# Kernel optimization log

Measured on AMD Instinct MI355X. Metric: run time of the kernel, lower is better.

## Reference

```python
import jax, jax.numpy as jnp
import numpy as np

LRELU_GAIN = np.sqrt(2.0).astype(np.float32)  # apply_activation gain for leaky_relu


def setup_inputs() -> dict:
    key = jax.random.key(0)
    ks = jax.random.split(key, 8)
    N, H, W, C_in = 8, 256, 256, 128
    num_ws, w_dim, fmaps, kernel = 16, 512, 128, 3
    return {
        "x": jax.random.normal(ks[0], (N, H, W, C_in), dtype=jnp.float32),
        "dlatents": jax.random.normal(ks[1], (N, num_ws, w_dim), dtype=jnp.float32),
        "noise": jax.random.normal(ks[2], (N, H, W, 1), dtype=jnp.float32),
        "affine_w": jax.random.normal(ks[3], (w_dim, C_in), dtype=jnp.float32),
        "affine_b": jnp.ones((C_in,), dtype=jnp.float32),  # bias_init=1
        "conv_w": jax.random.normal(ks[4], (kernel, kernel, C_in, fmaps), dtype=jnp.float32),
        "conv_b": jax.random.normal(ks[5], (fmaps,), dtype=jnp.float32),
        "noise_strength": jax.random.uniform(ks[6], (1,), dtype=jnp.float32),
        "layer_idx": 5,
    }


def reference(x, dlatents, noise, affine_w, affine_b, conv_w, conv_b, noise_strength, layer_idx):
    # --- affine (equalized-lr Linear, lr_multiplier=1): s = z @ (W/sqrt(fan_in)) + b ---
    w_dim = affine_w.shape[0]
    z = dlatents[:, layer_idx]                                   # [N, w_dim]
    s = z @ (affine_w * np.float32(1.0 / np.sqrt(w_dim))) + affine_b   # [N, C_in]

    # --- equalized-lr conv weight: w * 1/sqrt(k*k*C_in) ---
    k, _, cin, cout = conv_w.shape
    w = conv_w * np.float32(1.0 / np.sqrt(k * k * cin))          # [k,k,Cin,Cout]

    # --- demodulation coefficient d[n,o] = rsqrt(sum_{k,k,i} (w*s)^2 + eps) ---
    d = jax.lax.rsqrt(jnp.einsum('hwio,ni->no', jnp.square(w), jnp.square(s)) + 1e-8)  # [N, Cout]

    # --- non-fused modconv: modulate input, shared conv, demodulate output ---
    xm = x * s[:, None, None, :]                                 # [N,H,W,Cin]
    y = jax.lax.conv_general_dilated(
        xm, w, window_strides=(1, 1), padding='SAME',
        dimension_numbers=('NHWC', 'HWIO', 'NHWC'))              # [N,H,W,Cout]
    y = y * d[:, None, None, :]

    # --- noise injection, bias, activation (leaky_relu 0.2 with sqrt(2) gain) ---
    y = y + noise_strength[0] * noise
    y = y + conv_b
    return jax.nn.leaky_relu(y, negative_slope=0.2) * LRELU_GAIN
```

## Files before the change

### kernel.cpp

```cpp
#include <hip/hip_runtime.h>

typedef unsigned short u16;
typedef unsigned int   u32;
typedef __bf16 v8bf __attribute__((ext_vector_type(8)));
typedef float  v4f  __attribute__((ext_vector_type(4)));

#define INV_SQRT_W   0.044194173824159216f
#define INV_SQRT_KKC 0.029462782549439483f
#define LRELU_GAIN   1.4142135623730951f

__device__ __forceinline__ u16 f2bf(float f) {
    u32 u = __float_as_uint(f);
    u = (u + 0x7fffu + ((u >> 16) & 1u)) >> 16;
    return (u16)u;
}

__device__ __forceinline__ void glds16(const u16* g, u16* l) {
    __builtin_amdgcn_global_load_lds(
        (const __attribute__((address_space(1))) void*)g,
        (__attribute__((address_space(3))) void*)l, 16, 0, 0);
}

__global__ void k_s1(const float* __restrict__ dlat,
                     const float* __restrict__ aw,
                     const int*   __restrict__ lidx,
                     float* __restrict__ part)
{
    const int b   = blockIdx.x;
    const int n   = b >> 2, kh = b & 3;
    const int tid = threadIdx.x;
    const int i   = tid & 127, half = tid >> 7;
    const int li  = lidx[0];
    const float* z = dlat + (n * 16 + li) * 512 + kh * 128 + half * 64;
    const float* a = aw + (kh * 128 + half * 64) * 128 + i;
    float a0 = 0.f, a1 = 0.f;
    #pragma unroll 8
    for (int k = 0; k < 64; k += 2) {
        a0 += z[k]     * a[k * 128];
        a1 += z[k + 1] * a[(k + 1) * 128];
    }
    __shared__ float red[256];
    red[tid] = a0 + a1;
    __syncthreads();
    if (tid < 128)
        part[b * 128 + i] = red[i] + red[i + 128];
}

__global__ void k_s2(const float* __restrict__ part,
                     const float* __restrict__ ab,
                     float* __restrict__ s_out)
{
    const int n = blockIdx.x, i = threadIdx.x;
    float s = part[(n * 4 + 0) * 128 + i] + part[(n * 4 + 1) * 128 + i]
            + part[(n * 4 + 2) * 128 + i] + part[(n * 4 + 3) * 128 + i];
    s_out[n * 128 + i] = s * INV_SQRT_W + ab[i];
}

__global__ void k_w2(const float* __restrict__ cw, float* __restrict__ W2)
{
    const int idx = blockIdx.x * 256 + threadIdx.x;
    float acc = 0.f;
    #pragma unroll
    for (int t = 0; t < 9; ++t) {
        float w = cw[t * 16384 + idx];
        acc += w * w;
    }
    W2[idx] = acc * (INV_SQRT_KKC * INV_SQRT_KKC);
}

__global__ void k_d(const float* __restrict__ W2,
                    const float* __restrict__ s_buf,
                    float* __restrict__ d_out)
{
    const int n = blockIdx.x;
    const int o = threadIdx.x;
    __shared__ float s2[128];
    float sv = s_buf[n * 128 + o];
    s2[o] = sv * sv;
    __syncthreads();
    float acc = 1e-8f;
    #pragma unroll 4
    for (int i = 0; i < 128; ++i)
        acc += W2[i * 128 + o] * s2[i];
    d_out[n * 128 + o] = 1.0f / sqrtf(acc);
}

__global__ void k_wmod(const float* __restrict__ cw,
                       const float* __restrict__ s_buf,
                       const float* __restrict__ d_buf,
                       u16* __restrict__ wmod)
{
    const int b   = blockIdx.x;
    const int n   = b / 36;
    const int s   = b - n * 36;
    const int q4  = s / 9;
    const int r   = s - q4 * 9;
    const int tw  = r / 3, th = r - tw * 3;
    const int tap = th * 3 + tw;
    const int cibase = q4 * 32;
    const int tid = threadIdx.x;
    __shared__ float ssh[32], dsh[128];
    if (tid < 32)  ssh[tid] = s_buf[n * 128 + cibase + tid] * INV_SQRT_KKC;
    if (tid < 128) dsh[tid] = d_buf[n * 128 + tid];
    __syncthreads();
    u16* wt = wmod + ((size_t)b << 12);
    #pragma unroll
    for (int rep = 0; rep < 2; ++rep) {
        int t2   = rep * 256 + tid;
        int g    = t2 >> 7;
        int cout = t2 & 127;
        float dv = dsh[cout];
        u32 pk[4];
        #pragma unroll
        for (int jj = 0; jj < 4; ++jj) {
            int cl = g * 8 + jj * 2;
            float v0 = cw[((tap * 128 + cibase + cl) << 7) + cout]     * ssh[cl]     * dv;
            float v1 = cw[((tap * 128 + cibase + cl + 1) << 7) + cout] * ssh[cl + 1] * dv;
            pk[jj] = (u32)f2bf(v0) | ((u32)f2bf(v1) << 16);
        }
        *(uint4*)&wt[(g << 10) + (cout << 3)] = *(uint4*)pk;
    }
}

template<int T>
__device__ __forceinline__ void conv_step(const u16* __restrict__ wn,
                                          u16* __restrict__ bsh,
                                          const u16* a_base,
                                          const u16* b_lane,
                                          v8bf af[6], v4f acc[4][4],
                                          int wid, int lane)
{
    constexpr int q4 = T / 9, r = T % 9, tw = r / 3, th = r % 3;
    constexpr int slot = T % 3;
    constexpr int hq = q4 & 1;
    if constexpr (T == 0 || T == 18)
        asm volatile("s_waitcnt vmcnt(1) lgkmcnt(0)" ::: "memory");
    else if constexpr (T == 35)
        asm volatile("s_waitcnt vmcnt(0)" ::: "memory");
    else
        asm volatile("s_waitcnt vmcnt(1)" ::: "memory");
    __builtin_amdgcn_s_barrier();
    asm volatile("" ::: "memory");

    v8bf bf[4];
    #pragma unroll
    for (int ni = 0; ni < 4; ++ni)
        bf[ni] = *(const v8bf*)(b_lane + slot * 4096 + (ni << 7));
    if constexpr (th == 0) {
        #pragma unroll
        for (int j = 0; j < 6; ++j)
            af[j] = *(const v8bf*)(a_base + hq * 10400 + (j * 18 + tw) * 8);
    }
    if constexpr (T + 2 < 36) {
        constexpr int ns = (T + 2) % 3;
        glds16(wn + (T + 2) * 4096 + (wid << 9) + (lane << 3),
               &bsh[ns * 4096 + (wid << 9) + (lane << 3)]);
    }
    #pragma unroll
    for (int mi = 0; mi < 4; ++mi)
        #pragma unroll
        for (int ni = 0; ni < 4; ++ni)
            acc[mi][ni] = __builtin_amdgcn_mfma_f32_16x16x32_bf16(
                af[mi + th], bf[ni], acc[mi][ni], 0, 0, 0);
}

__global__ __launch_bounds__(512, 4) void k_conv(
    const float* __restrict__ x,
    const float* __restrict__ noise,
    const float* __restrict__ conv_b,
    const float* __restrict__ nstr,
    const u16*   __restrict__ wmod,
    float* __restrict__ out)
{
    __shared__ __align__(16) u16 xs[20800];
    __shared__ __align__(16) u16 bsh[12288];

    const int bid0 = blockIdx.x;
    const int bid  = ((bid0 & 7) << 8) + (bid0 >> 3);
    const int n   = bid >> 8;
    const int hb  = (bid >> 4) & 15;
    const int wb  = bid & 15;
    const int h0  = hb << 4, w0 = wb << 4;

    const int tid  = threadIdx.x;
    const int lane = tid & 63;
    const int wid  = tid >> 6;
    const int wm   = wid >> 1;
    const int wn_  = wid & 1;
    const int lr   = lane & 15;
    const int kg   = lane >> 4;

    const float* xbase = x + ((size_t)n << 16) * 128;

    #define STAGE_X(ph)                                                              \
    for (int t = tid; t < 2592; t += 512) {                                          \
        int q = t >> 3, g = t & 7;                                                   \
        int rr_ = q / 18, cc = q - rr_ * 18;                                         \
        int gh = h0 + rr_ - 1, gw = w0 + cc - 1;                                     \
        float v0=0.f,v1=0.f,v2=0.f,v3=0.f,v4=0.f,v5=0.f,v6=0.f,v7=0.f;               \
        if ((unsigned)gh < 256u && (unsigned)gw < 256u) {                            \
            const float* src = xbase + (size_t)((gh << 8) + gw) * 128                \
                               + (ph) * 64 + (g << 3);                               \
            float4 fa = *(const float4*)(src);                                       \
            float4 fb = *(const float4*)(src + 4);                                   \
            v0=fa.x; v1=fa.y; v2=fa.z; v3=fa.w; v4=fb.x; v5=fb.y; v6=fb.z; v7=fb.w;  \
        }                                                                            \
        v8bf pk;                                                                     \
        pk[0]=(__bf16)v0; pk[1]=(__bf16)v1; pk[2]=(__bf16)v2; pk[3]=(__bf16)v3;      \
        pk[4]=(__bf16)v4; pk[5]=(__bf16)v5; pk[6]=(__bf16)v6; pk[7]=(__bf16)v7;      \
        *(v8bf*)&xs[g * 2600 + q * 8] = pk;                                          \
    }

    STAGE_X(0)

    const u16* wn = wmod + ((size_t)n * 36) * 4096;
    #pragma unroll
    for (int s0 = 0; s0 < 2; ++s0)
        glds16(wn + s0 * 4096 + (wid << 9) + (lane << 3),
               &bsh[s0 * 4096 + (wid << 9) + (lane << 3)]);

    v4f acc[4][4];
    #pragma unroll
    for (int a = 0; a < 4; ++a)
        #pragma unroll
        for (int b2 = 0; b2 < 4; ++b2) {
            v4f zz = {0.f, 0.f, 0.f, 0.f};
            acc[a][b2] = zz;
        }

    const u16* const a_base = &xs[kg * 2600 + (wm * 72 + lr) * 8];
    const u16* const b_lane = &bsh[kg * 1024 + (wn_ * 64 + lr) * 8];

    v8bf af[6];
    conv_step< 0>(wn, bsh, a_base, b_lane, af, acc, wid, lane);
    conv_step< 1>(wn, bsh, a_base, b_lane, af, acc, wid, lane);
    conv_step< 2>(wn, bsh, a_base, b_lane, af, acc, wid, lane);
    conv_step< 3>(wn, bsh, a_base, b_lane, af, acc, wid, lane);
    conv_step< 4>(wn, bsh, a_base, b_lane, af, acc, wid, lane);
    conv_step< 5>(wn, bsh, a_base, b_lane, af, acc, wid, lane);
    conv_step< 6>(wn, bsh, a_base, b_lane, af, acc, wid, lane);
    conv_step< 7>(wn, bsh, a_base, b_lane, af, acc, wid, lane);
    conv_step< 8>(wn, bsh, a_base, b_lane, af, acc, wid, lane);
    conv_step< 9>(wn, bsh, a_base, b_lane, af, acc, wid, lane);
    conv_step<10>(wn, bsh, a_base, b_lane, af, acc, wid, lane);
    conv_step<11>(wn, bsh, a_base, b_lane, af, acc, wid, lane);
    conv_step<12>(wn, bsh, a_base, b_lane, af, acc, wid, lane);
    conv_step<13>(wn, bsh, a_base, b_lane, af, acc, wid, lane);
    conv_step<14>(wn, bsh, a_base, b_lane, af, acc, wid, lane);
    conv_step<15>(wn, bsh, a_base, b_lane, af, acc, wid, lane);
    conv_step<16>(wn, bsh, a_base, b_lane, af, acc, wid, lane);
    conv_step<17>(wn, bsh, a_base, b_lane, af, acc, wid, lane);

    STAGE_X(1)

    conv_step<18>(wn, bsh, a_base, b_lane, af, acc, wid, lane);
    conv_step<19>(wn, bsh, a_base, b_lane, af, acc, wid, lane);
    conv_step<20>(wn, bsh, a_base, b_lane, af, acc, wid, lane);
    conv_step<21>(wn, bsh, a_base, b_lane, af, acc, wid, lane);
    conv_step<22>(wn, bsh, a_base, b_lane, af, acc, wid, lane);
    conv_step<23>(wn, bsh, a_base, b_lane, af, acc, wid, lane);
    conv_step<24>(wn, bsh, a_base, b_lane, af, acc, wid, lane);
    conv_step<25>(wn, bsh, a_base, b_lane, af, acc, wid, lane);
    conv_step<26>(wn, bsh, a_base, b_lane, af, acc, wid, lane);
    conv_step<27>(wn, bsh, a_base, b_lane, af, acc, wid, lane);
    conv_step<28>(wn, bsh, a_base, b_lane, af, acc, wid, lane);
    conv_step<29>(wn, bsh, a_base, b_lane, af, acc, wid, lane);
    conv_step<30>(wn, bsh, a_base, b_lane, af, acc, wid, lane);
    conv_step<31>(wn, bsh, a_base, b_lane, af, acc, wid, lane);
    conv_step<32>(wn, bsh, a_base, b_lane, af, acc, wid, lane);
    conv_step<33>(wn, bsh, a_base, b_lane, af, acc, wid, lane);
    conv_step<34>(wn, bsh, a_base, b_lane, af, acc, wid, lane);
    conv_step<35>(wn, bsh, a_base, b_lane, af, acc, wid, lane);

    const float ns = nstr[0];
    float cb4[4];
    #pragma unroll
    for (int ni = 0; ni < 4; ++ni)
        cb4[ni] = conv_b[wn_ * 64 + ni * 16 + lr];
    #pragma unroll
    for (int mi = 0; mi < 4; ++mi) {
        const int h = h0 + wm * 4 + mi;
        #pragma unroll
        for (int j = 0; j < 4; ++j) {
            const int w  = w0 + kg * 4 + j;
            const float nz = noise[((n << 8) + h) * 256 + w] * ns;
            float* orow = out + (size_t)((((n << 8) + h) << 8) + w) * 128;
            #pragma unroll
            for (int ni = 0; ni < 4; ++ni) {
                const int cout = wn_ * 64 + ni * 16 + lr;
                float v = acc[mi][ni][j] + nz + cb4[ni];
                v = (v < 0.f ? 0.2f * v : v) * LRELU_GAIN;
                orow[cout] = v;
            }
        }
    }
}

extern "C" void kernel_launch(void* const* d_in, const int* in_sizes, int n_in,
                              void* d_out, int out_size, void* d_ws, size_t ws_size,
                              hipStream_t stream) {
    const float* x     = (const float*)d_in[0];
    const float* dlat  = (const float*)d_in[1];
    const float* noise = (const float*)d_in[2];
    const float* aw    = (const float*)d_in[3];
    const float* ab    = (const float*)d_in[4];
    const float* cw    = (const float*)d_in[5];
    const float* cb    = (const float*)d_in[6];
    const float* nstr  = (const float*)d_in[7];
    const int*   lidx  = (const int*)d_in[8];
    float* out = (float*)d_out;

    float* s_buf = (float*)d_ws;
    float* d_buf = (float*)((char*)d_ws + 4096);
    float* W2    = (float*)((char*)d_ws + 8192);
    u16*   wmod  = (u16*)((char*)d_ws + 8192);
    float* part  = (float*)((char*)d_ws + 8192 + 2359296);

    k_w2  <<<64,  256, 0, stream>>>(cw, W2);
    k_s1  <<<32,  256, 0, stream>>>(dlat, aw, lidx, part);
    k_s2  <<<8,   128, 0, stream>>>(part, ab, s_buf);
    k_d   <<<8,   128, 0, stream>>>(W2, s_buf, d_buf);
    k_wmod<<<288, 256, 0, stream>>>(cw, s_buf, d_buf, wmod);
    k_conv<<<2048,512, 0, stream>>>(x, noise, cb, nstr, wmod, out);
}
```

Baseline: 195.0 us.

## Prefetch next stage's LDS fragments before barrier and raise MFMA priority

Restructures the conv main loop so each step issues its global-to-LDS weight prefetch, runs the MFMAs at raised wave priority, then waits, barriers and loads the next stage's A/B fragments into registers. The goal is to take the LDS reads and the barrier off the critical path just before the MFMAs, so matrix work overlaps fragment loading. The prologue now issues three weight stages, one of which is loaded again redundantly by step 0, and barriers are placed explicitly around the x restaging. The waitcnt bookkeeping is more delicate, and holding the next stage's fragments in registers during the MFMAs raises register pressure.

Measured after the change: 197.2 us. No clear change (+1.2%).

```diff
diff --git a/kernel.cpp b/kernel.cpp
--- a/kernel.cpp
+++ b/kernel.cpp
@@ -122,27 +122,14 @@
     }
 }
 
-template<int T>
-__device__ __forceinline__ void conv_step(const u16* __restrict__ wn,
-                                          u16* __restrict__ bsh,
-                                          const u16* a_base,
-                                          const u16* b_lane,
-                                          v8bf af[6], v4f acc[4][4],
-                                          int wid, int lane)
-{
-    constexpr int q4 = T / 9, r = T % 9, tw = r / 3, th = r % 3;
-    constexpr int slot = T % 3;
-    constexpr int hq = q4 & 1;
-    if constexpr (T == 0 || T == 18)
-        asm volatile("s_waitcnt vmcnt(1) lgkmcnt(0)" ::: "memory");
-    else if constexpr (T == 35)
-        asm volatile("s_waitcnt vmcnt(0)" ::: "memory");
-    else
-        asm volatile("s_waitcnt vmcnt(1)" ::: "memory");
-    __builtin_amdgcn_s_barrier();
-    asm volatile("" ::: "memory");
-
-    v8bf bf[4];
+template<int S>
+__device__ __forceinline__ void read_stage(const u16* __restrict__ b_lane,
+                                           const u16* __restrict__ a_base,
+                                           v8bf bf[4], v8bf af[6])
+{
+    constexpr int slot = S % 3;
+    constexpr int r = S % 9, tw = r / 3, th = r % 3;
+    constexpr int hq = (S / 9) & 1;
     #pragma unroll
     for (int ni = 0; ni < 4; ++ni)
         bf[ni] = *(const v8bf*)(b_lane + slot * 4096 + (ni << 7));
@@ -151,17 +138,41 @@
         for (int j = 0; j < 6; ++j)
             af[j] = *(const v8bf*)(a_base + hq * 10400 + (j * 18 + tw) * 8);
     }
+}
+
+template<int T, bool DO_TAIL>
+__device__ __forceinline__ void conv_step(const u16* __restrict__ wn,
+                                          u16* __restrict__ bsh,
+                                          const u16* __restrict__ a_base,
+                                          const u16* __restrict__ b_lane,
+                                          v8bf af[6], v8bf bf[4],
+                                          v4f acc[4][4],
+                                          int wid, int lane)
+{
+    constexpr int th = (T % 9) % 3;
     if constexpr (T + 2 < 36) {
         constexpr int ns = (T + 2) % 3;
         glds16(wn + (T + 2) * 4096 + (wid << 9) + (lane << 3),
                &bsh[ns * 4096 + (wid << 9) + (lane << 3)]);
     }
+    asm volatile("s_waitcnt lgkmcnt(0)" ::: "memory");
+    __builtin_amdgcn_s_setprio(1);
     #pragma unroll
     for (int mi = 0; mi < 4; ++mi)
         #pragma unroll
         for (int ni = 0; ni < 4; ++ni)
             acc[mi][ni] = __builtin_amdgcn_mfma_f32_16x16x32_bf16(
                 af[mi + th], bf[ni], acc[mi][ni], 0, 0, 0);
+    __builtin_amdgcn_s_setprio(0);
+    if constexpr (DO_TAIL) {
+        if constexpr (T + 2 < 36)
+            asm volatile("s_waitcnt vmcnt(1)" ::: "memory");
+        else
+            asm volatile("s_waitcnt vmcnt(0)" ::: "memory");
+        __builtin_amdgcn_s_barrier();
+        asm volatile("" ::: "memory");
+        read_stage<T + 1>(b_lane, a_base, bf, af);
+    }
 }
 
 __global__ __launch_bounds__(512, 4) void k_conv(
@@ -215,7 +226,7 @@
 
     const u16* wn = wmod + ((size_t)n * 36) * 4096;
     #pragma unroll
-    for (int s0 = 0; s0 < 2; ++s0)
+    for (int s0 = 0; s0 < 3; ++s0)
         glds16(wn + s0 * 4096 + (wid << 9) + (lane << 3),
                &bsh[s0 * 4096 + (wid << 9) + (lane << 3)]);
 
@@ -231,46 +242,59 @@
     const u16* const a_base = &xs[kg * 2600 + (wm * 72 + lr) * 8];
     const u16* const b_lane = &bsh[kg * 1024 + (wn_ * 64 + lr) * 8];
 
-    v8bf af[6];
-    conv_step< 0>(wn, bsh, a_base, b_lane, af, acc, wid, lane);
-    conv_step< 1>(wn, bsh, a_base, b_lane, af, acc, wid, lane);
-    conv_step< 2>(wn, bsh, a_base, b_lane, af, acc, wid, lane);
-    conv_step< 3>(wn, bsh, a_base, b_lane, af, acc, wid, lane);
-    conv_step< 4>(wn, bsh, a_base, b_lane, af, acc, wid, lane);
-    conv_step< 5>(wn, bsh, a_base, b_lane, af, acc, wid, lane);
-    conv_step< 6>(wn, bsh, a_base, b_lane, af, acc, wid, lane);
-    conv_step< 7>(wn, bsh, a_base, b_lane, af, acc, wid, lane);
-    conv_step< 8>(wn, bsh, a_base, b_lane, af, acc, wid, lane);
-    conv_step< 9>(wn, bsh, a_base, b_lane, af, acc, wid, lane);
-    conv_step<10>(wn, bsh, a_base, b_lane, af, acc, wid, lane);
-    conv_step<11>(wn, bsh, a_base, b_lane, af, acc, wid, lane);
-    conv_step<12>(wn, bsh, a_base, b_lane, af, acc, wid, lane);
-    conv_step<13>(wn, bsh, a_base, b_lane, af, acc, wid, lane);
-    conv_step<14>(wn, bsh, a_base, b_lane, af, acc, wid, lane);
-    conv_step<15>(wn, bsh, a_base, b_lane, af, acc, wid, lane);
-    conv_step<16>(wn, bsh, a_base, b_lane, af, acc, wid, lane);
-    conv_step<17>(wn, bsh, a_base, b_lane, af, acc, wid, lane);
+    asm volatile("s_waitcnt vmcnt(2) lgkmcnt(0)" ::: "memory");
+    __builtin_amdgcn_s_barrier();
+    asm volatile("" ::: "memory");
+    v8bf af[6], bf[4];
+    read_stage<0>(b_lane, a_base, bf, af);
+
+    conv_step< 0, true >(wn, bsh, a_base, b_lane, af, bf, acc, wid, lane);
+    conv_step< 1, true >(wn, bsh, a_base, b_lane, af, bf, acc, wid, lane);
+    conv_step< 2, true >(wn, bsh, a_base, b_lane, af, bf, acc, wid, lane);
+    conv_step< 3, true >(wn, bsh, a_base, b_lane, af, bf, acc, wid, lane);
+    conv_step< 4, true >(wn, bsh, a_base, b_lane, af, bf, acc, wid, lane);
+    conv_step< 5, true >(wn, bsh, a_base, b_lane, af, bf, acc, wid, lane);
+    conv_step< 6, true >(wn, bsh, a_base, b_lane, af, bf, acc, wid, lane);
+    conv_step< 7, true >(wn, bsh, a_base, b_lane, af, bf, acc, wid, lane);
+    conv_step< 8, true >(wn, bsh, a_base, b_lane, af, bf, acc, wid, lane);
+    conv_step< 9, true >(wn, bsh, a_base, b_lane, af, bf, acc, wid, lane);
+    conv_step<10, true >(wn, bsh, a_base, b_lane, af, bf, acc, wid, lane);
+    conv_step<11, true >(wn, bsh, a_base, b_lane, af, bf, acc, wid, lane);
+    conv_step<12, true >(wn, bsh, a_base, b_lane, af, bf, acc, wid, lane);
+    conv_step<13, true >(wn, bsh, a_base, b_lane, af, bf, acc, wid, lane);
+    conv_step<14, true >(wn, bsh, a_base, b_lane, af, bf, acc, wid, lane);
+    conv_step<15, true >(wn, bsh, a_base, b_lane, af, bf, acc, wid, lane);
+    conv_step<16, true >(wn, bsh, a_base, b_lane, af, bf, acc, wid, lane);
+    conv_step<17, false>(wn, bsh, a_base, b_lane, af, bf, acc, wid, lane);
+    asm volatile("s_waitcnt vmcnt(1)" ::: "memory");
+    __builtin_amdgcn_s_barrier();
+    asm volatile("" ::: "memory");
 
     STAGE_X(1)
 
-    conv_step<18>(wn, bsh, a_base, b_lane, af, acc, wid, lane);
-    conv_step<19>(wn, bsh, a_base, b_lane, af, acc, wid, lane);
-    conv_step<20>(wn, bsh, a_base, b_lane, af, acc, wid, lane);
-    conv_step<21>(wn, bsh, a_base, b_lane, af, acc, wid, lane);
-    conv_step<22>(wn, bsh, a_base, b_lane, af, acc, wid, lane);
-    conv_step<23>(wn, bsh, a_base, b_lane, af, acc, wid, lane);
-    conv_step<24>(wn, bsh, a_base, b_lane, af, acc, wid, lane);
-    conv_step<25>(wn, bsh, a_base, b_lane, af, acc, wid, lane);
-    conv_step<26>(wn, bsh, a_base, b_lane, af, acc, wid, lane);
-    conv_step<27>(wn, bsh, a_base, b_lane, af, acc, wid, lane);
-    conv_step<28>(wn, bsh, a_base, b_lane, af, acc, wid, lane);
-    conv_step<29>(wn, bsh, a_base, b_lane, af, acc, wid, lane);
-    conv_step<30>(wn, bsh, a_base, b_lane, af, acc, wid, lane);
-    conv_step<31>(wn, bsh, a_base, b_lane, af, acc, wid, lane);
-    conv_step<32>(wn, bsh, a_base, b_lane, af, acc, wid, lane);
-    conv_step<33>(wn, bsh, a_base, b_lane, af, acc, wid, lane);
-    conv_step<34>(wn, bsh, a_base, b_lane, af, acc, wid, lane);
-    conv_step<35>(wn, bsh, a_base, b_lane, af, acc, wid, lane);
+    asm volatile("s_waitcnt lgkmcnt(0)" ::: "memory");
+    __builtin_amdgcn_s_barrier();
+    asm volatile("" ::: "memory");
+    read_stage<18>(b_lane, a_base, bf, af);
+
+    conv_step<18, true >(wn, bsh, a_base, b_lane, af, bf, acc, wid, lane);
+    conv_step<19, true >(wn, bsh, a_base, b_lane, af, bf, acc, wid, lane);
+    conv_step<20, true >(wn, bsh, a_base, b_lane, af, bf, acc, wid, lane);
+    conv_step<21, true >(wn, bsh, a_base, b_lane, af, bf, acc, wid, lane);
+    conv_step<22, true >(wn, bsh, a_base, b_lane, af, bf, acc, wid, lane);
+    conv_step<23, true >(wn, bsh, a_base, b_lane, af, bf, acc, wid, lane);
+    conv_step<24, true >(wn, bsh, a_base, b_lane, af, bf, acc, wid, lane);
+    conv_step<25, true >(wn, bsh, a_base, b_lane, af, bf, acc, wid, lane);
+    conv_step<26, true >(wn, bsh, a_base, b_lane, af, bf, acc, wid, lane);
+    conv_step<27, true >(wn, bsh, a_base, b_lane, af, bf, acc, wid, lane);
+    conv_step<28, true >(wn, bsh, a_base, b_lane, af, bf, acc, wid, lane);
+    conv_step<29, true >(wn, bsh, a_base, b_lane, af, bf, acc, wid, lane);
+    conv_step<30, true >(wn, bsh, a_base, b_lane, af, bf, acc, wid, lane);
+    conv_step<31, true >(wn, bsh, a_base, b_lane, af, bf, acc, wid, lane);
+    conv_step<32, true >(wn, bsh, a_base, b_lane, af, bf, acc, wid, lane);
+    conv_step<33, true >(wn, bsh, a_base, b_lane, af, bf, acc, wid, lane);
+    conv_step<34, true >(wn, bsh, a_base, b_lane, af, bf, acc, wid, lane);
+    conv_step<35, false>(wn, bsh, a_base, b_lane, af, bf, acc, wid, lane);
 
     const float ns = nstr[0];
     float cb4[4];
```
